# Kernel optimization log

Measured on AMD Instinct MI355X. Metric: run time of the kernel, lower is better.

Reference implementation:

```python
import jax, jax.numpy as jnp
import numpy as np

N = 50000          # nodes
E = 800000         # edges (avg degree 16)
H, D = 4, 32       # heads, per-head channels; hidden = H*D = 128
DIMS_IN = [32, 128, 128]


def setup_inputs() -> dict:
    key = jax.random.key(0)
    ks = jax.random.split(key, 40)
    inp = {}
    inp["x"] = jax.random.normal(ks[0], (N, 32), jnp.float32)
    inp["edge_index"] = jax.random.randint(ks[1], (2, E), 0, N, dtype=jnp.int32)
    i = 2
    for l, din in enumerate(DIMS_IN):
        for nm in ["q", "k", "v", "s"]:
            inp[f"W{nm}{l}"] = jax.random.normal(ks[i], (din, H * D), jnp.float32) / np.float32(np.sqrt(din)); i += 1
            inp[f"b{nm}{l}"] = jax.random.normal(ks[i], (H * D,), jnp.float32) * 0.01; i += 1
    inp["Wf"] = jax.random.normal(ks[i], (H * D, 1), jnp.float32) / np.float32(np.sqrt(H * D)); i += 1
    inp["bf"] = jax.random.normal(ks[i], (1,), jnp.float32) * 0.01
    return inp


def _transformer_conv(x, src, dst, Wq, bq, Wk, bk, Wv, bv, Ws, bs):
    """PyG TransformerConv (concat=True, root_weight=True, beta=False, eval mode)."""
    n = x.shape[0]
    q = (x @ Wq + bq).reshape(n, H, D)   # queries at nodes
    k = (x @ Wk + bk).reshape(n, H, D)
    v = (x @ Wv + bv).reshape(n, H, D)
    # per-edge attention score: q at destination, k at source
    s = jnp.einsum("ehd,ehd->eh", q[dst], k[src]) / np.float32(np.sqrt(D))  # [E,H]
    # segment softmax over incoming edges of each destination node
    m = jax.ops.segment_max(s, dst, num_segments=n)          # [N,H]
    e = jnp.exp(s - m[dst])                                  # [E,H]
    den = jax.ops.segment_sum(e, dst, num_segments=n)        # [N,H]
    alpha = e / den[dst]                                     # [E,H]
    agg = jax.ops.segment_sum(alpha[:, :, None] * v[src], dst, num_segments=n)  # [N,H,D]
    return agg.reshape(n, H * D) + (x @ Ws + bs)             # skip connection


def reference(x, edge_index,
              Wq0, bq0, Wk0, bk0, Wv0, bv0, Ws0, bs0,
              Wq1, bq1, Wk1, bk1, Wv1, bv1, Ws1, bs1,
              Wq2, bq2, Wk2, bk2, Wv2, bv2, Ws2, bs2,
              Wf, bf):
    src, dst = edge_index[0], edge_index[1]
    layers = [
        (Wq0, bq0, Wk0, bk0, Wv0, bv0, Ws0, bs0),
        (Wq1, bq1, Wk1, bk1, Wv1, bv1, Ws1, bs1),
        (Wq2, bq2, Wk2, bk2, Wv2, bv2, Ws2, bs2),
    ]
    h = x
    for p in layers:
        h = jax.nn.relu(_transformer_conv(h, src, dst, *p))
    out = jax.nn.sigmoid(h @ Wf + bf)  # [N,1]
    return out
```

## Files before the change

### kernel.cpp

```cpp
#include <hip/hip_runtime.h>
#include <hip/hip_bf16.h>
#include <cstdint>
#include <cstddef>

typedef __attribute__((ext_vector_type(8))) short bf16x8;
typedef __attribute__((ext_vector_type(4))) float f32x4;
typedef __attribute__((ext_vector_type(2))) float f32x2;

__device__ __forceinline__ unsigned short f2bs(float f){
  __hip_bfloat16 h = __float2bfloat16(f);
  return *(unsigned short*)&h;
}
__device__ __forceinline__ float bflo(unsigned int u){ return __uint_as_float(u << 16); }
__device__ __forceinline__ float bfhi(unsigned int u){ return __uint_as_float(u & 0xffff0000u); }
__device__ __forceinline__ f32x2 b2f2(unsigned int u){
  return (f32x2){ __uint_as_float(u << 16), __uint_as_float(u & 0xffff0000u) };
}

__global__ void hist_kernel(const int* __restrict__ dst, int E, int* __restrict__ deg){
  int e = blockIdx.x*256 + threadIdx.x;
  if (e < E) atomicAdd(&deg[dst[e]], 1);
}

__global__ __launch_bounds__(1024)
void scanA_kernel(const int* __restrict__ deg, int n, int* __restrict__ rowptr, int* __restrict__ bsums){
  __shared__ int s[1024];
  int t = threadIdx.x;
  int i = blockIdx.x*1024 + t;
  int v = (i < n) ? deg[i] : 0;
  s[t] = v;
  __syncthreads();
  #pragma unroll
  for (int off = 1; off < 1024; off <<= 1){
    int a = (t >= off) ? s[t-off] : 0;
    __syncthreads();
    s[t] += a;
    __syncthreads();
  }
  if (i < n) rowptr[i] = s[t] - v;
  if (t == 1023) bsums[blockIdx.x] = s[1023];
}

__global__ __launch_bounds__(1024)
void scanC_kernel(const int* __restrict__ bsums, int nch, int n,
                  int* __restrict__ rowptr, int* __restrict__ cursor){
  __shared__ int choff_s;
  int t = threadIdx.x;
  if (t < 64){
    int v = (t < nch && t < (int)blockIdx.x) ? bsums[t] : 0;
    #pragma unroll
    for (int off = 1; off <= 32; off <<= 1) v += __shfl_xor(v, off, 64);
    if (t == 0) choff_s = v;
  }
  __syncthreads();
  int i = blockIdx.x*1024 + t;
  if (i < n){
    int r = rowptr[i] + choff_s;
    rowptr[i] = r;
    cursor[i] = r;
  }
}

__global__ void scatter_kernel(const int* __restrict__ src, const int* __restrict__ dst, int E,
                               int* __restrict__ cursor, int* __restrict__ adj){
  int e = blockIdx.x*256 + threadIdx.x;
  if (e < E){
    int pos = atomicAdd(&cursor[dst[e]], 1);
    adj[pos] = src[e];
  }
}

struct PrepArgs {
  const float* w[12];
  unsigned short* o[12];
  const float* x;
  unsigned short* xb;
  int n2;
};

__global__ void prep_kernel(PrepArgs a){
  int m = blockIdx.y;
  if (m < 12){
    int K = (m < 4) ? 32 : 128;
    int halfK = K >> 1;
    int tot = 128 * halfK;
    int e = blockIdx.x*256 + threadIdx.x;
    if (e >= tot) return;
    int n  = e / halfK;
    int k2 = e % halfK;
    const float* W = a.w[m];
    unsigned int lo = __float_as_uint(W[(2*k2)  *128 + n]) >> 16;
    unsigned int hi = __float_as_uint(W[(2*k2+1)*128 + n]) & 0xffff0000u;
    ((unsigned int*)a.o[m])[e] = lo | hi;
  } else {
    for (int i = blockIdx.x*256 + threadIdx.x; i < a.n2; i += 32*256){
      float2 v = ((const float2*)a.x)[i];
      ((unsigned int*)a.xb)[i] = (__float_as_uint(v.x) >> 16) | (__float_as_uint(v.y) & 0xffff0000u);
    }
  }
}

template<int DIN>
__global__ __launch_bounds__(256)
void gemm4_mfma(const unsigned short* __restrict__ X, int nn,
                const unsigned short* __restrict__ T0, const unsigned short* __restrict__ T1,
                const unsigned short* __restrict__ T2, const unsigned short* __restrict__ T3,
                const float* __restrict__ b0, const float* __restrict__ b1,
                const float* __restrict__ b2, const float* __restrict__ b3,
                unsigned short* __restrict__ O0, unsigned short* __restrict__ O1,
                unsigned short* __restrict__ O2, unsigned short* __restrict__ O3)
{
  constexpr int KP = DIN + 8;
  __shared__ __align__(16) unsigned short wt[128*KP];
  int t = threadIdx.x;
  int msel = blockIdx.y;
  const unsigned short* WT = (msel==0)?T0:(msel==1)?T1:(msel==2)?T2:T3;
  const float* B = (msel==0)?b0:(msel==1)?b1:(msel==2)?b2:b3;
  unsigned short* O = (msel==0)?O0:(msel==1)?O1:(msel==2)?O2:O3;

  {
    const int NU = 128*DIN/8;
    for (int u = t; u < NU; u += 256){
      uint4 v = ((const uint4*)WT)[u];
      int n = u / (DIN/8), b = u % (DIN/8);
      *(uint4*)&wt[n*KP + b*8] = v;
    }
  }

  int lane = t & 63, wv = t >> 6;
  int m0 = blockIdx.x*64 + wv*16;
  int n16 = lane & 15, quad = lane >> 4;

  bf16x8 af[DIN/32];
  {
    const unsigned short* xrow = X + (size_t)(m0 + n16)*DIN + quad*8;
    #pragma unroll
    for (int s = 0; s < DIN/32; s++) af[s] = *(const bf16x8*)(xrow + s*32);
  }

  __syncthreads();

  f32x4 acc[8];
  #pragma unroll
  for (int c=0;c<8;c++) acc[c] = (f32x4){0.f,0.f,0.f,0.f};

  #pragma unroll
  for (int s = 0; s < DIN/32; s++){
    #pragma unroll
    for (int c = 0; c < 8; c++){
      bf16x8 bf = *(const bf16x8*)&wt[(c*16 + n16)*KP + s*32 + quad*8];
      acc[c] = __builtin_amdgcn_mfma_f32_16x16x32_bf16(af[s], bf, acc[c], 0, 0, 0);
    }
  }

  #pragma unroll
  for (int c = 0; c < 8; c++){
    int col = c*16 + n16;
    float bias = B[col];
    #pragma unroll
    for (int r = 0; r < 4; r++){
      int row = m0 + quad*4 + r;
      if (row < nn) O[(size_t)row*128 + col] = f2bs(acc[c][r] + bias);
    }
  }
}

template<bool FINAL>
__global__ __launch_bounds__(256)
void attn_kernel(const unsigned short* __restrict__ q,  const unsigned short* __restrict__ kmat,
                 const unsigned short* __restrict__ vmat, const unsigned short* __restrict__ skip,
                 const int* __restrict__ rowptr, const int* __restrict__ deg,
                 const int* __restrict__ adj, unsigned short* __restrict__ hout,
                 const float* __restrict__ Wf, const float* __restrict__ bfp,
                 float* __restrict__ out, int nn)
{
  int lane = threadIdx.x & 63, wid = threadIdx.x >> 6;
  int n = blockIdx.x*4 + wid;
  if (n >= nn) return;
  int p = lane & 15, g = lane >> 4;
  const float RS = 0.17677669529663687f;

  f32x2 qv[4];
  { uint4 qu = *(const uint4*)(q + (size_t)n*128 + p*8);
    qv[0]=b2f2(qu.x); qv[1]=b2f2(qu.y); qv[2]=b2f2(qu.z); qv[3]=b2f2(qu.w); }

  int start = rowptr[n], dg = deg[n];
  float m = -INFINITY, l = 0.f;
  f32x2 acc[4] = {{0.f,0.f},{0.f,0.f},{0.f,0.f},{0.f,0.f}};

  for (int c0 = 0; c0 < dg; c0 += 64){
    int cn = min(64, dg - c0);
    int idx = adj[start + c0 + min(lane, cn-1)];
    int nit = (cn + 7) >> 3;

    bool a0 = 2*g < cn, a1 = 2*g + 1 < cn;
    int s0 = __shfl(idx, min(2*g    , cn-1), 64);
    int s1 = __shfl(idx, min(2*g + 1, cn-1), 64);
    uint4 ku0 = *(const uint4*)(kmat + (size_t)s0*128 + p*8);
    uint4 ku1 = *(const uint4*)(kmat + (size_t)s1*128 + p*8);
    uint4 vu0 = *(const uint4*)(vmat + (size_t)s0*128 + p*8);
    uint4 vu1 = *(const uint4*)(vmat + (size_t)s1*128 + p*8);

    for (int it = 0; it < nit; ++it){
      int jn0 = (it+1)*8 + 2*g;
      bool b0 = jn0 < cn, b1 = jn0 + 1 < cn;
      int t0 = __shfl(idx, min(jn0    , cn-1), 64);
      int t1 = __shfl(idx, min(jn0 + 1, cn-1), 64);
      uint4 kn0={0,0,0,0}, kn1={0,0,0,0}, vn0={0,0,0,0}, vn1={0,0,0,0};
      if (it + 1 < nit){
        kn0 = *(const uint4*)(kmat + (size_t)t0*128 + p*8);
        kn1 = *(const uint4*)(kmat + (size_t)t1*128 + p*8);
        vn0 = *(const uint4*)(vmat + (size_t)t0*128 + p*8);
        vn1 = *(const uint4*)(vmat + (size_t)t1*128 + p*8);
      }
      f32x2 d0v = qv[0]*b2f2(ku0.x);
      d0v = __builtin_elementwise_fma(qv[1], b2f2(ku0.y), d0v);
      d0v = __builtin_elementwise_fma(qv[2], b2f2(ku0.z), d0v);
      d0v = __builtin_elementwise_fma(qv[3], b2f2(ku0.w), d0v);
      f32x2 d1v = qv[0]*b2f2(ku1.x);
      d1v = __builtin_elementwise_fma(qv[1], b2f2(ku1.y), d1v);
      d1v = __builtin_elementwise_fma(qv[2], b2f2(ku1.z), d1v);
      d1v = __builtin_elementwise_fma(qv[3], b2f2(ku1.w), d1v);
      float d0 = d0v.x + d0v.y;
      float d1 = d1v.x + d1v.y;
      d0 += __shfl_xor(d0, 1, 64); d0 += __shfl_xor(d0, 2, 64);
      d1 += __shfl_xor(d1, 1, 64); d1 += __shfl_xor(d1, 2, 64);
      float f0 = a0 ? d0*RS : -INFINITY;
      float f1 = a1 ? d1*RS : -INFINITY;

      float nm = fmaxf(m, fmaxf(f0, f1));
      float r  = __expf(fmaxf(m  - nm, -80.f));
      float w0 = __expf(fmaxf(f0 - nm, -80.f));
      float w1 = __expf(fmaxf(f1 - nm, -80.f));
      m = nm;
      l = l*r + (w0 + w1);
      f32x2 rr  = {r , r };
      f32x2 w0v = {w0, w0};
      f32x2 w1v = {w1, w1};
      acc[0] = __builtin_elementwise_fma(w1v, b2f2(vu1.x),
               __builtin_elementwise_fma(w0v, b2f2(vu0.x), acc[0]*rr));
      acc[1] = __builtin_elementwise_fma(w1v, b2f2(vu1.y),
               __builtin_elementwise_fma(w0v, b2f2(vu0.y), acc[1]*rr));
      acc[2] = __builtin_elementwise_fma(w1v, b2f2(vu1.z),
               __builtin_elementwise_fma(w0v, b2f2(vu0.z), acc[2]*rr));
      acc[3] = __builtin_elementwise_fma(w1v, b2f2(vu1.w),
               __builtin_elementwise_fma(w0v, b2f2(vu0.w), acc[3]*rr));
      ku0=kn0; ku1=kn1; vu0=vn0; vu1=vn1; a0=b0; a1=b1;
    }
  }

  float m1 = fmaxf(m, __shfl_xor(m, 16, 64));
  float M  = fmaxf(m1, __shfl_xor(m1, 32, 64));
  float sc = __expf(fmaxf(m - M, -80.f));
  float lp = l * sc;
  lp += __shfl_xor(lp, 16, 64);
  float L = lp + __shfl_xor(lp, 32, 64);
  f32x2 scv = {sc, sc};
  float o[8];
  #pragma unroll
  for (int i=0;i<4;i++){
    f32x2 a = acc[i]*scv;
    a.x += __shfl_xor(a.x, 16, 64); a.y += __shfl_xor(a.y, 16, 64);
    a.x += __shfl_xor(a.x, 32, 64); a.y += __shfl_xor(a.y, 32, 64);
    o[2*i] = a.x; o[2*i+1] = a.y;
  }
  float inv = (L > 0.f) ? 1.f/L : 0.f;
  float sk[8];
  { uint4 su = *(const uint4*)(skip + (size_t)n*128 + p*8);
    sk[0]=bflo(su.x); sk[1]=bfhi(su.x); sk[2]=bflo(su.y); sk[3]=bfhi(su.y);
    sk[4]=bflo(su.z); sk[5]=bfhi(su.z); sk[6]=bflo(su.w); sk[7]=bfhi(su.w); }
  #pragma unroll
  for (int i=0;i<8;i++) o[i] = fmaxf(fmaf(o[i], inv, sk[i]), 0.f);

  if constexpr (!FINAL){
    if (g == 0){
      uint4 st;
      st.x = (unsigned)f2bs(o[0]) | ((unsigned)f2bs(o[1])<<16);
      st.y = (unsigned)f2bs(o[2]) | ((unsigned)f2bs(o[3])<<16);
      st.z = (unsigned)f2bs(o[4]) | ((unsigned)f2bs(o[5])<<16);
      st.w = (unsigned)f2bs(o[6]) | ((unsigned)f2bs(o[7])<<16);
      *(uint4*)(hout + (size_t)n*128 + p*8) = st;
    }
  } else {
    float4 w0 = *(const float4*)(Wf + p*8);
    float4 w1 = *(const float4*)(Wf + p*8 + 4);
    float pd = o[0]*w0.x;
    pd = fmaf(o[1], w0.y, pd); pd = fmaf(o[2], w0.z, pd); pd = fmaf(o[3], w0.w, pd);
    pd = fmaf(o[4], w1.x, pd); pd = fmaf(o[5], w1.y, pd);
    pd = fmaf(o[6], w1.z, pd); pd = fmaf(o[7], w1.w, pd);
    pd += __shfl_xor(pd, 1, 64);
    pd += __shfl_xor(pd, 2, 64);
    pd += __shfl_xor(pd, 4, 64);
    pd += __shfl_xor(pd, 8, 64);
    if (lane == 0){
      float z = pd + bfp[0];
      out[n] = 1.f / (1.f + __expf(-z));
    }
  }
}

extern "C" void kernel_launch(void* const* d_in, const int* in_sizes, int n_in,
                              void* d_out, int out_size, void* d_ws, size_t ws_size,
                              hipStream_t stream) {
  const int N = in_sizes[0] / 32;
  const int E = in_sizes[1] / 2;
  const float* x = (const float*)d_in[0];
  const int* ei  = (const int*)d_in[1];
  const int* src = ei;
  const int* dst = ei + E;
  auto Wp = [&](int i){ return (const float*)d_in[i]; };
  const int NP = N + 64;

  char* p = (char*)d_ws;
  auto alloc = [&](size_t b){ char* r = p; p += (b + 255) & ~(size_t)255; return (void*)r; };
  unsigned short* F0 = (unsigned short*)alloc((size_t)NP*128*2);
  unsigned short* F1 = (unsigned short*)alloc((size_t)NP*128*2);
  unsigned short* Qb = (unsigned short*)alloc((size_t)NP*128*2);
  unsigned short* Kb = (unsigned short*)alloc((size_t)NP*128*2);
  unsigned short* Vb = (unsigned short*)alloc((size_t)NP*128*2);
  unsigned short* xb = (unsigned short*)alloc((size_t)NP*32*2);
  unsigned short* WT[12];
  for (int i = 0; i < 12; i++){
    int K = (i < 4) ? 32 : 128;
    WT[i] = (unsigned short*)alloc((size_t)128*K*2);
  }
  int* deg    = (int*)alloc((size_t)N*4);
  int* rowptr = (int*)alloc((size_t)N*4);
  int* cursor = (int*)alloc((size_t)N*4);
  int* adj    = (int*)alloc((size_t)E*4);
  int* bsums  = (int*)alloc(64*4);

  hipMemsetAsync(deg, 0, (size_t)N*4, stream);
  hist_kernel<<<(E+255)/256, 256, 0, stream>>>(dst, E, deg);
  int nch = (N + 1023) / 1024;
  scanA_kernel<<<nch, 1024, 0, stream>>>(deg, N, rowptr, bsums);
  scanC_kernel<<<nch, 1024, 0, stream>>>(bsums, nch, N, rowptr, cursor);
  scatter_kernel<<<(E+255)/256, 256, 0, stream>>>(src, dst, E, cursor, adj);

  PrepArgs pa;
  const int widx[12] = {2,4,6,8, 10,12,14,16, 18,20,22,24};
  for (int i = 0; i < 12; i++){ pa.w[i] = Wp(widx[i]); pa.o[i] = WT[i]; }
  pa.x = x; pa.xb = xb; pa.n2 = N*16;
  prep_kernel<<<dim3(32,13), 256, 0, stream>>>(pa);

  dim3 gg((N+63)/64, 4);
  int ab = (N + 3) / 4;
  gemm4_mfma<32><<<gg, 256, 0, stream>>>(xb, N,
      WT[0],WT[1],WT[2],WT[3], Wp(3),Wp(5),Wp(7),Wp(9), Qb,Kb,Vb, F0);
  attn_kernel<false><<<ab, 256, 0, stream>>>(Qb,Kb,Vb, F0, rowptr,deg,adj, F0,
      nullptr, nullptr, nullptr, N);
  gemm4_mfma<128><<<gg, 256, 0, stream>>>(F0, N,
      WT[4],WT[5],WT[6],WT[7], Wp(11),Wp(13),Wp(15),Wp(17), Qb,Kb,Vb, F1);
  attn_kernel<false><<<ab, 256, 0, stream>>>(Qb,Kb,Vb, F1, rowptr,deg,adj, F1,
      nullptr, nullptr, nullptr, N);
  gemm4_mfma<128><<<gg, 256, 0, stream>>>(F1, N,
      WT[8],WT[9],WT[10],WT[11], Wp(19),Wp(21),Wp(23),Wp(25), Qb,Kb,Vb, F0);
  attn_kernel<true><<<ab, 256, 0, stream>>>(Qb,Kb,Vb, F0, rowptr,deg,adj, nullptr,
      Wp(26), Wp(27), (float*)d_out, N);
}
```

Measured before the change: 485.5 us.

## Interleave K and V rows and compute all four projections per GEMM block

```diff
diff --git a/kernel.cpp b/kernel.cpp
--- a/kernel.cpp
+++ b/kernel.cpp
@@ -15,6 +15,11 @@
 __device__ __forceinline__ float bfhi(unsigned int u){ return __uint_as_float(u & 0xffff0000u); }
 __device__ __forceinline__ f32x2 b2f2(unsigned int u){
   return (f32x2){ __uint_as_float(u << 16), __uint_as_float(u & 0xffff0000u) };
+}
+
+__global__ void zero_int_kernel(int* __restrict__ p, int n){
+  int i = blockIdx.x*256 + threadIdx.x;
+  if (i < n) p[i] = 0;
 }
 
 __global__ void hist_kernel(const int* __restrict__ dst, int E, int* __restrict__ deg){
@@ -102,31 +107,17 @@
 
 template<int DIN>
 __global__ __launch_bounds__(256)
-void gemm4_mfma(const unsigned short* __restrict__ X, int nn,
-                const unsigned short* __restrict__ T0, const unsigned short* __restrict__ T1,
-                const unsigned short* __restrict__ T2, const unsigned short* __restrict__ T3,
-                const float* __restrict__ b0, const float* __restrict__ b1,
-                const float* __restrict__ b2, const float* __restrict__ b3,
-                unsigned short* __restrict__ O0, unsigned short* __restrict__ O1,
-                unsigned short* __restrict__ O2, unsigned short* __restrict__ O3)
+void gemm4_fused(const unsigned short* __restrict__ X, int nn,
+                 const unsigned short* __restrict__ T0, const unsigned short* __restrict__ T1,
+                 const unsigned short* __restrict__ T2, const unsigned short* __restrict__ T3,
+                 const float* __restrict__ b0, const float* __restrict__ b1,
+                 const float* __restrict__ b2, const float* __restrict__ b3,
+                 unsigned short* __restrict__ Q, unsigned short* __restrict__ KV,
+                 unsigned short* __restrict__ S)
 {
   constexpr int KP = DIN + 8;
   __shared__ __align__(16) unsigned short wt[128*KP];
   int t = threadIdx.x;
-  int msel = blockIdx.y;
-  const unsigned short* WT = (msel==0)?T0:(msel==1)?T1:(msel==2)?T2:T3;
-  const float* B = (msel==0)?b0:(msel==1)?b1:(msel==2)?b2:b3;
-  unsigned short* O = (msel==0)?O0:(msel==1)?O1:(msel==2)?O2:O3;
-
-  {
-    const int NU = 128*DIN/8;
-    for (int u = t; u < NU; u += 256){
-      uint4 v = ((const uint4*)WT)[u];
-      int n = u / (DIN/8), b = u % (DIN/8);
-      *(uint4*)&wt[n*KP + b*8] = v;
-    }
-  }
-
   int lane = t & 63, wv = t >> 6;
   int m0 = blockIdx.x*64 + wv*16;
   int n16 = lane & 15, quad = lane >> 4;
@@ -138,37 +129,56 @@
     for (int s = 0; s < DIN/32; s++) af[s] = *(const bf16x8*)(xrow + s*32);
   }
 
-  __syncthreads();
-
-  f32x4 acc[8];
+  const unsigned short* Ts[4] = {T0, T1, T2, T3};
+  const float*          Bs[4] = {b0, b1, b2, b3};
+
   #pragma unroll
-  for (int c=0;c<8;c++) acc[c] = (f32x4){0.f,0.f,0.f,0.f};
-
-  #pragma unroll
-  for (int s = 0; s < DIN/32; s++){
+  for (int msel = 0; msel < 4; msel++){
+    __syncthreads();
+    {
+      const unsigned short* WT = Ts[msel];
+      const int NU = 128*DIN/8;
+      for (int u = t; u < NU; u += 256){
+        uint4 v = ((const uint4*)WT)[u];
+        int n = u / (DIN/8), b = u % (DIN/8);
+        *(uint4*)&wt[n*KP + b*8] = v;
+      }
+    }
+    __syncthreads();
+
+    f32x4 acc[8];
+    #pragma unroll
+    for (int c=0;c<8;c++) acc[c] = (f32x4){0.f,0.f,0.f,0.f};
+    #pragma unroll
+    for (int s = 0; s < DIN/32; s++){
+      #pragma unroll
+      for (int c = 0; c < 8; c++){
+        bf16x8 bf = *(const bf16x8*)&wt[(c*16 + n16)*KP + s*32 + quad*8];
+        acc[c] = __builtin_amdgcn_mfma_f32_16x16x32_bf16(af[s], bf, acc[c], 0, 0, 0);
+      }
+    }
+
+    unsigned short* O = (msel==0) ? Q : (msel==3) ? S : KV;
+    int ostride = (msel==1 || msel==2) ? 256 : 128;
+    int ooff    = (msel==2) ? 128 : 0;
+    const float* B = Bs[msel];
     #pragma unroll
     for (int c = 0; c < 8; c++){
-      bf16x8 bf = *(const bf16x8*)&wt[(c*16 + n16)*KP + s*32 + quad*8];
-      acc[c] = __builtin_amdgcn_mfma_f32_16x16x32_bf16(af[s], bf, acc[c], 0, 0, 0);
-    }
-  }
-
-  #pragma unroll
-  for (int c = 0; c < 8; c++){
-    int col = c*16 + n16;
-    float bias = B[col];
-    #pragma unroll
-    for (int r = 0; r < 4; r++){
-      int row = m0 + quad*4 + r;
-      if (row < nn) O[(size_t)row*128 + col] = f2bs(acc[c][r] + bias);
+      int col = c*16 + n16;
+      float bias = B[col];
+      #pragma unroll
+      for (int r = 0; r < 4; r++){
+        int row = m0 + quad*4 + r;
+        if (row < nn) O[(size_t)row*ostride + ooff + col] = f2bs(acc[c][r] + bias);
+      }
     }
   }
 }
 
 template<bool FINAL>
 __global__ __launch_bounds__(256)
-void attn_kernel(const unsigned short* __restrict__ q,  const unsigned short* __restrict__ kmat,
-                 const unsigned short* __restrict__ vmat, const unsigned short* __restrict__ skip,
+void attn_kernel(const unsigned short* __restrict__ q,  const unsigned short* __restrict__ kv,
+                 const unsigned short* __restrict__ skip,
                  const int* __restrict__ rowptr, const int* __restrict__ deg,
                  const int* __restrict__ adj, unsigned short* __restrict__ hout,
                  const float* __restrict__ Wf, const float* __restrict__ bfp,
@@ -196,10 +206,10 @@
     bool a0 = 2*g < cn, a1 = 2*g + 1 < cn;
     int s0 = __shfl(idx, min(2*g    , cn-1), 64);
     int s1 = __shfl(idx, min(2*g + 1, cn-1), 64);
-    uint4 ku0 = *(const uint4*)(kmat + (size_t)s0*128 + p*8);
-    uint4 ku1 = *(const uint4*)(kmat + (size_t)s1*128 + p*8);
-    uint4 vu0 = *(const uint4*)(vmat + (size_t)s0*128 + p*8);
-    uint4 vu1 = *(const uint4*)(vmat + (size_t)s1*128 + p*8);
+    uint4 ku0 = *(const uint4*)(kv + (size_t)s0*256 + p*8);
+    uint4 ku1 = *(const uint4*)(kv + (size_t)s1*256 + p*8);
+    uint4 vu0 = *(const uint4*)(kv + (size_t)s0*256 + 128 + p*8);
+    uint4 vu1 = *(const uint4*)(kv + (size_t)s1*256 + 128 + p*8);
 
     for (int it = 0; it < nit; ++it){
       int jn0 = (it+1)*8 + 2*g;
@@ -208,10 +218,10 @@
       int t1 = __shfl(idx, min(jn0 + 1, cn-1), 64);
       uint4 kn0={0,0,0,0}, kn1={0,0,0,0}, vn0={0,0,0,0}, vn1={0,0,0,0};
       if (it + 1 < nit){
-        kn0 = *(const uint4*)(kmat + (size_t)t0*128 + p*8);
-        kn1 = *(const uint4*)(kmat + (size_t)t1*128 + p*8);
-        vn0 = *(const uint4*)(vmat + (size_t)t0*128 + p*8);
-        vn1 = *(const uint4*)(vmat + (size_t)t1*128 + p*8);
+        kn0 = *(const uint4*)(kv + (size_t)t0*256 + p*8);
+        kn1 = *(const uint4*)(kv + (size_t)t1*256 + p*8);
+        vn0 = *(const uint4*)(kv + (size_t)t0*256 + 128 + p*8);
+        vn1 = *(const uint4*)(kv + (size_t)t1*256 + 128 + p*8);
       }
       f32x2 d0v = qv[0]*b2f2(ku0.x);
       d0v = __builtin_elementwise_fma(qv[1], b2f2(ku0.y), d0v);
@@ -313,12 +323,11 @@
 
   char* p = (char*)d_ws;
   auto alloc = [&](size_t b){ char* r = p; p += (b + 255) & ~(size_t)255; return (void*)r; };
-  unsigned short* F0 = (unsigned short*)alloc((size_t)NP*128*2);
-  unsigned short* F1 = (unsigned short*)alloc((size_t)NP*128*2);
-  unsigned short* Qb = (unsigned short*)alloc((size_t)NP*128*2);
-  unsigned short* Kb = (unsigned short*)alloc((size_t)NP*128*2);
-  unsigned short* Vb = (unsigned short*)alloc((size_t)NP*128*2);
-  unsigned short* xb = (unsigned short*)alloc((size_t)NP*32*2);
+  unsigned short* F0  = (unsigned short*)alloc((size_t)NP*128*2);
+  unsigned short* F1  = (unsigned short*)alloc((size_t)NP*128*2);
+  unsigned short* Qb  = (unsigned short*)alloc((size_t)NP*128*2);
+  unsigned short* KVb = (unsigned short*)alloc((size_t)NP*256*2);
+  unsigned short* xb  = (unsigned short*)alloc((size_t)NP*32*2);
   unsigned short* WT[12];
   for (int i = 0; i < 12; i++){
     int K = (i < 4) ? 32 : 128;
@@ -330,7 +339,7 @@
   int* adj    = (int*)alloc((size_t)E*4);
   int* bsums  = (int*)alloc(64*4);
 
-  hipMemsetAsync(deg, 0, (size_t)N*4, stream);
+  zero_int_kernel<<<(N+255)/256, 256, 0, stream>>>(deg, N);
   hist_kernel<<<(E+255)/256, 256, 0, stream>>>(dst, E, deg);
   int nch = (N + 1023) / 1024;
   scanA_kernel<<<nch, 1024, 0, stream>>>(deg, N, rowptr, bsums);
@@ -343,18 +352,18 @@
   pa.x = x; pa.xb = xb; pa.n2 = N*16;
   prep_kernel<<<dim3(32,13), 256, 0, stream>>>(pa);
 
-  dim3 gg((N+63)/64, 4);
+  int gb = (N + 63) / 64;
   int ab = (N + 3) / 4;
-  gemm4_mfma<32><<<gg, 256, 0, stream>>>(xb, N,
-      WT[0],WT[1],WT[2],WT[3], Wp(3),Wp(5),Wp(7),Wp(9), Qb,Kb,Vb, F0);
-  attn_kernel<false><<<ab, 256, 0, stream>>>(Qb,Kb,Vb, F0, rowptr,deg,adj, F0,
+  gemm4_fused<32><<<gb, 256, 0, stream>>>(xb, N,
+      WT[0],WT[1],WT[2],WT[3], Wp(3),Wp(5),Wp(7),Wp(9), Qb, KVb, F0);
+  attn_kernel<false><<<ab, 256, 0, stream>>>(Qb, KVb, F0, rowptr,deg,adj, F0,
       nullptr, nullptr, nullptr, N);
-  gemm4_mfma<128><<<gg, 256, 0, stream>>>(F0, N,
-      WT[4],WT[5],WT[6],WT[7], Wp(11),Wp(13),Wp(15),Wp(17), Qb,Kb,Vb, F1);
-  attn_kernel<false><<<ab, 256, 0, stream>>>(Qb,Kb,Vb, F1, rowptr,deg,adj, F1,
+  gemm4_fused<128><<<gb, 256, 0, stream>>>(F0, N,
+      WT[4],WT[5],WT[6],WT[7], Wp(11),Wp(13),Wp(15),Wp(17), Qb, KVb, F1);
+  attn_kernel<false><<<ab, 256, 0, stream>>>(Qb, KVb, F1, rowptr,deg,adj, F1,
       nullptr, nullptr, nullptr, N);
-  gemm4_mfma<128><<<gg, 256, 0, stream>>>(F1, N,
-      WT[8],WT[9],WT[10],WT[11], Wp(19),Wp(21),Wp(23),Wp(25), Qb,Kb,Vb, F0);
-  attn_kernel<true><<<ab, 256, 0, stream>>>(Qb,Kb,Vb, F0, rowptr,deg,adj, nullptr,
+  gemm4_fused<128><<<gb, 256, 0, stream>>>(F1, N,
+      WT[8],WT[9],WT[10],WT[11], Wp(19),Wp(21),Wp(23),Wp(25), Qb, KVb, F0);
+  attn_kernel<true><<<ab, 256, 0, stream>>>(Qb, KVb, F0, rowptr,deg,adj, nullptr,
       Wp(26), Wp(27), (float*)d_out, N);
 }
```

New measurement: 500.9 us. 3.2% more time.
